# Kernel optimization log

Measured on AMD Instinct MI355X. Metric: run time of the kernel, lower is better.

Reference implementation:

```python
import jax, jax.numpy as jnp
import numpy as np
import math

QUERY_LEN = 64
VALUES_LEN = 64
NUM_HEADS = 16


def setup_inputs() -> dict:
    key = jax.random.key(0)
    k1, k2, k3, k4 = jax.random.split(key, 4)
    B, G, N = 2, 4, 1024
    D = QUERY_LEN * NUM_HEADS  # 1024
    queries = jax.random.normal(k1, (B, G, N, D), dtype=jnp.float32)
    keys = jax.random.normal(k2, (B, G, N, D), dtype=jnp.float32)
    values = jax.random.normal(k3, (B, G, N, VALUES_LEN * NUM_HEADS), dtype=jnp.float32)
    neuron_bank_connectivity_sub = jax.random.uniform(k4, (1, G, 1, N, N), dtype=jnp.float32)
    return {
        "queries": queries,
        "keys": keys,
        "values": values,
        "neuron_bank_connectivity_sub": neuron_bank_connectivity_sub,
    }


def reference(queries, keys, values, neuron_bank_connectivity_sub):
    B, G, N, _ = queries.shape
    H, dq, dv = NUM_HEADS, QUERY_LEN, VALUES_LEN
    # view last dim as (vec_len, num_heads), move heads forward: [B,G,H,N,d]
    q = queries.reshape(B, G, N, dq, H).transpose(0, 1, 4, 2, 3)
    k = keys.reshape(B, G, N, dq, H).transpose(0, 1, 4, 2, 3)
    v = values.reshape(B, G, N, dv, H).transpose(0, 1, 4, 2, 3)
    scores = jnp.einsum('bghnd,bghmd->bghnm', q, k) / math.sqrt(dq)
    probs = jax.nn.softmax(scores - neuron_bank_connectivity_sub, axis=-1)
    out = jnp.einsum('bghnm,bghmd->bghnd', probs, v)  # [B,G,H,N,dv]
    # Faithful to original: view() applied to the contiguous [B,G,H,N,dv] buffer
    return out.reshape(B, G, N, H * dv)
```

## Files before the change

### kernel.cpp

```cpp
#include <hip/hip_runtime.h>
#include <hip/hip_bf16.h>
#include <math.h>

#define B_ 2
#define G_ 4
#define N_ 1024
#define H_ 16
#define D_ 64
#define BG_ (B_*G_)
#define BGH_ (B_*G_*H_)
#define MK 64
#define LOG2E 1.44269504f
#define QSCALE (0.125f * LOG2E)

typedef __bf16 bf16;
typedef bf16 bf16x8 __attribute__((ext_vector_type(8)));
typedef bf16 bf16x2 __attribute__((ext_vector_type(2)));
typedef float f32x4 __attribute__((ext_vector_type(4)));
typedef float f32x16 __attribute__((ext_vector_type(16)));
typedef int i32x4 __attribute__((ext_vector_type(4)));
typedef unsigned u32x2 __attribute__((ext_vector_type(2)));

static __device__ __forceinline__ f32x16 mfma32(bf16x8 a, bf16x8 b, f32x16 c) {
    return __builtin_amdgcn_mfma_f32_32x32x16_bf16(a, b, c, 0, 0, 0);
}

static __device__ __forceinline__ unsigned pk2(float a, float b) {
    bf16x2 t; t[0] = (bf16)a; t[1] = (bf16)b;
    return __builtin_bit_cast(unsigned, t);
}

static __device__ __forceinline__ void pl32swap(unsigned& a, unsigned& b, int hi) {
#if __has_builtin(__builtin_amdgcn_permlane32_swap)
    u32x2 r = __builtin_amdgcn_permlane32_swap(a, b, false, false);
    a = r[0]; b = r[1];
    (void)hi;
#else
    unsigned ax = (unsigned)__shfl_xor((int)a, 32, 64);
    unsigned bx = (unsigned)__shfl_xor((int)b, 32, 64);
    unsigned na = hi ? bx : a;
    unsigned nb = hi ? b : ax;
    a = na; b = nb;
#endif
}

static __device__ __forceinline__ void gll16(const void* gsrc, void* ldst, int lane) {
#if __has_builtin(__builtin_amdgcn_global_load_lds)
    (void)lane;
    __builtin_amdgcn_global_load_lds((const __attribute__((address_space(1))) void*)gsrc,
                                     (__attribute__((address_space(3))) void*)ldst, 16, 0, 0);
#else
    *(bf16x8*)((bf16*)ldst + lane * 8) = *(const bf16x8*)((const bf16*)gsrc);
#endif
}

#define HS 1160
#define NS 72

__global__ __launch_bounds__(256) void transpose_fused(
    const float* __restrict__ q, const float* __restrict__ k, const float* __restrict__ v,
    const float* __restrict__ bias,
    bf16* __restrict__ qt, bf16* __restrict__ ktb, bf16* __restrict__ vtT16,
    float* __restrict__ biasX)
{
    __shared__ __attribute__((aligned(16))) bf16 lds[16 * HS];
    int bx = blockIdx.x;
    int t = threadIdx.x;

    if (bx >= 3 * 512) {
        int idx = bx - 3 * 512;
        int gg  = idx >> 8;
        int tl  = idx & 255;
        int q0  = (tl >> 4) * 64;
        int m0  = (tl & 15) * 64;
        float* ldsF = (float*)lds;

        int mi = t & 15, qr = t >> 4;
#pragma unroll
        for (int rr = 0; rr < 4; ++rr) {
            int row = qr + rr * 16;
            f32x4 val = *(const f32x4*)(bias + ((size_t)(gg * N_ + q0 + row) * N_ + m0 + 4 * mi));
            *(f32x4*)(&ldsF[row * 68 + 4 * mi]) = val;
        }
        __syncthreads();
        int qr2 = t & 63, mb0 = t >> 6;
#pragma unroll
        for (int kk = 0; kk < 4; ++kk) {
            int mbi = mb0 + kk * 4;
            f32x4 vv = *(const f32x4*)(&ldsF[qr2 * 68 + 4 * mbi]);
            *(f32x4*)(biasX + (((size_t)gg * 256 + m0 / 4 + mbi) * N_ + q0 + qr2) * 4) = vv;
        }
        return;
    }

    int tensor = bx >> 9;
    int rr = bx & 511;
    int bg = rr >> 6;
    int tile = rr & 63;
    int n0 = tile * 16;

    const float* src = (tensor == 0) ? q : (tensor == 1) ? k : v;
    float scale = (tensor == 0) ? QSCALE : 1.0f;
    const float* sb = src + (size_t)bg * N_ * 1024 + (size_t)n0 * 1024;

    int h0 = 4 * (t & 3);
    int d  = t >> 2;
    int wbase = h0 * HS + d;
#pragma unroll 4
    for (int i = 0; i < 16; ++i) {
        float4 val = ((const float4*)(sb + (size_t)i * 1024))[t];
        bf16* p = &lds[wbase + i * NS];
        p[0]        = (bf16)(val.x * scale);
        p[HS]       = (bf16)(val.y * scale);
        p[2 * HS]   = (bf16)(val.z * scale);
        p[3 * HS]   = (bf16)(val.w * scale);
    }
    __syncthreads();

    if (tensor < 2) {
        bf16* dst = (tensor == 0) ? qt : ktb;
        int n  = (t >> 3) & 15;
        int db = t & 7;
        int hb = t >> 7;
#pragma unroll
        for (int i = 0; i < 8; ++i) {
            int h = 2 * i + hb;
            bf16x8 vv = *(const bf16x8*)(&lds[h * HS + n * NS + db * 8]);
            *(bf16x8*)(dst + (((size_t)(bg * H_ + h)) * N_ + n0 + n) * D_ + db * 8) = vv;
        }
    } else {
        int dd = t & 63;
        int hb = t >> 6;
#pragma unroll
        for (int i = 0; i < 4; ++i) {
            int h = hb * 4 + i;
            bf16x8 v0, v1;
#pragma unroll
            for (int jj = 0; jj < 8; ++jj) v0[jj] = lds[h * HS + jj * NS + dd];
#pragma unroll
            for (int jj = 0; jj < 8; ++jj) v1[jj] = lds[h * HS + (8 + jj) * NS + dd];
            bf16* dst = vtT16 + (((size_t)(bg * H_ + h) * 64 + tile) * D_ + dd) * 16;
            *(bf16x8*)dst       = v0;
            *(bf16x8*)(dst + 8) = v1;
        }
    }
}

__global__ __launch_bounds__(256, 3) void flash_kernel(
    const bf16* __restrict__ qt, const bf16* __restrict__ kt, const bf16* __restrict__ vtT16,
    const float* __restrict__ biasX, float* __restrict__ out)
{
    __shared__ __attribute__((aligned(16))) bf16 k_lds[2][MK][D_];
    __shared__ __attribute__((aligned(16))) bf16 v_lds[2][D_][MK];

    int tid  = threadIdx.x;
    int w    = tid >> 6;
    int lane = tid & 63;
    int hi   = lane >> 5;
    int q31  = lane & 31;
    int key8 = (q31 & 7) << 3;
    int hi8  = hi << 3;

    int wg   = blockIdx.x;
    int xcd  = wg & 7;
    int slot = wg >> 3;
    int bgh  = xcd * 16 + (slot >> 3);
    int n0   = (slot & 7) * 128;
    int g    = (bgh >> 4) & (G_ - 1);

    const bf16* qb_base = qt + ((size_t)bgh * N_ + n0 + w * 32 + q31) * D_ + hi * 8;
    bf16x8 qb[4];
#pragma unroll
    for (int c = 0; c < 4; ++c) qb[c] = *(const bf16x8*)(qb_base + c * 16);

    f32x16 acc0 = {0,0,0,0,0,0,0,0,0,0,0,0,0,0,0,0};
    f32x16 acc1 = {0,0,0,0,0,0,0,0,0,0,0,0,0,0,0,0};
    float l = 0.f;

    int rloc = lane >> 3;
    int c16  = lane & 7;
    int csw  = c16 ^ rloc;
    bool isK = (w < 2);
    int wrow = (w & 1) * 32;
    const bf16* ksrc = kt + (size_t)bgh * N_ * D_ + (size_t)(wrow + rloc) * D_ + csw * 8;
    const bf16* vsrc = vtT16 + (((size_t)bgh * 64 + (csw >> 1)) * D_ + (wrow + rloc)) * 16 + (csw & 1) * 8;

    const float* bb = biasX + (size_t)g * (256u * 1024 * 4) + (size_t)(n0 + w * 32 + q31) * 4;

    if (isK) {
#pragma unroll
        for (int i = 0; i < 4; ++i) gll16(ksrc + (size_t)i * 8 * D_, &k_lds[0][wrow + i * 8][0], lane);
    } else {
#pragma unroll
        for (int i = 0; i < 4; ++i) gll16(vsrc + (size_t)i * 128, &v_lds[0][wrow + i * 8][0], lane);
    }
    f32x4 bnx[8];
#pragma unroll
    for (int tt = 0; tt < 2; ++tt)
#pragma unroll
        for (int u = 0; u < 4; ++u)
            bnx[tt * 4 + u] = *(const f32x4*)(bb + (size_t)(tt * 8 + 2 * u + hi) * 4096);

    for (int it = 0; it < N_ / MK; ++it) {
        int  cur  = it & 1;
        bool more = (it + 1 < N_ / MK);
        __syncthreads();

        if (more) {
            int nxt = cur ^ 1;
            if (isK) {
                const bf16* ks = ksrc + (size_t)(it + 1) * MK * D_;
#pragma unroll
                for (int i = 0; i < 4; ++i) gll16(ks + (size_t)i * 8 * D_, &k_lds[nxt][wrow + i * 8][0], lane);
            } else {
                const bf16* vs = vsrc + (size_t)(it + 1) * 4096;
#pragma unroll
                for (int i = 0; i < 4; ++i) gll16(vs + (size_t)i * 128, &v_lds[nxt][wrow + i * 8][0], lane);
            }
        }

        f32x16 s0 = {0,0,0,0,0,0,0,0,0,0,0,0,0,0,0,0};
        f32x16 s1 = {0,0,0,0,0,0,0,0,0,0,0,0,0,0,0,0};
        __builtin_amdgcn_s_setprio(1);
#pragma unroll
        for (int c = 0; c < 4; ++c) {
            int off = ((c << 4) | hi8) ^ key8;
            bf16x8 kb0 = *(const bf16x8*)(&k_lds[cur][q31][off]);
            bf16x8 kb1 = *(const bf16x8*)(&k_lds[cur][32 + q31][off]);
            s0 = mfma32(kb0, qb[c], s0);
            s1 = mfma32(kb1, qb[c], s1);
        }
        __builtin_amdgcn_s_setprio(0);

        unsigned wa[2][4], wb[2][4];
#pragma unroll
        for (int tt = 0; tt < 2; ++tt) {
#pragma unroll
            for (int u = 0; u < 4; ++u) {
                const f32x16& s = tt ? s1 : s0;
                f32x4 bvv = bnx[tt * 4 + u];
                float p0 = __builtin_amdgcn_exp2f(__builtin_fmaf(-LOG2E, bvv[0], s[4*u+0]));
                float p1 = __builtin_amdgcn_exp2f(__builtin_fmaf(-LOG2E, bvv[1], s[4*u+1]));
                float p2 = __builtin_amdgcn_exp2f(__builtin_fmaf(-LOG2E, bvv[2], s[4*u+2]));
                float p3 = __builtin_amdgcn_exp2f(__builtin_fmaf(-LOG2E, bvv[3], s[4*u+3]));
                l += (p0 + p1) + (p2 + p3);
                wa[tt][u] = pk2(p0, p1);
                wb[tt][u] = pk2(p2, p3);
            }
        }

        if (more) {
#pragma unroll
            for (int tt = 0; tt < 2; ++tt)
#pragma unroll
                for (int u = 0; u < 4; ++u)
                    bnx[tt * 4 + u] = *(const f32x4*)(bb + (size_t)((it + 1) * 16 + tt * 8 + 2 * u + hi) * 4096);
        }

#pragma unroll
        for (int tt = 0; tt < 2; ++tt) {
            pl32swap(wa[tt][0], wa[tt][1], hi);
            pl32swap(wb[tt][0], wb[tt][1], hi);
            pl32swap(wa[tt][2], wa[tt][3], hi);
            pl32swap(wb[tt][2], wb[tt][3], hi);
        }

        __builtin_amdgcn_s_setprio(1);
#pragma unroll
        for (int tt = 0; tt < 2; ++tt)
#pragma unroll
            for (int c01 = 0; c01 < 2; ++c01) {
                int kc = tt * 2 + c01;
                i32x4 bwi = { (int)wa[tt][2*c01], (int)wb[tt][2*c01],
                              (int)wa[tt][2*c01+1], (int)wb[tt][2*c01+1] };
                bf16x8 pb = __builtin_bit_cast(bf16x8, bwi);
                int off = ((kc << 4) | hi8) ^ key8;
                bf16x8 va0 = *(const bf16x8*)(&v_lds[cur][q31][off]);
                bf16x8 va1 = *(const bf16x8*)(&v_lds[cur][32 + q31][off]);
                acc0 = mfma32(va0, pb, acc0);
                acc1 = mfma32(va1, pb, acc1);
            }
        __builtin_amdgcn_s_setprio(0);
    }

    l += __shfl_xor(l, 32, 64);
    float inv = 1.0f / l;

    float* ob = out + ((size_t)bgh * N_ + n0 + w * 32 + q31) * D_ + hi * 4;
#pragma unroll
    for (int td = 0; td < 2; ++td) {
        const f32x16& a = td ? acc1 : acc0;
#pragma unroll
        for (int u = 0; u < 4; ++u) {
            f32x4 o = { a[4*u+0] * inv, a[4*u+1] * inv, a[4*u+2] * inv, a[4*u+3] * inv };
            *(f32x4*)(ob + td * 32 + u * 8) = o;
        }
    }
}

__global__ __launch_bounds__(256) void naive_kernel(
    const float* __restrict__ q, const float* __restrict__ k,
    const float* __restrict__ v, const float* __restrict__ bias,
    float* __restrict__ out)
{
    __shared__ float sc[N_];
    __shared__ float red[256];
    __shared__ float qrow[64];
    int n = blockIdx.x;
    int bgh = blockIdx.y;
    int bg = bgh >> 4, h = bgh & 15;
    int g = bg & (G_ - 1);
    int tid = threadIdx.x;
    const float* qr = q + ((size_t)(bg * N_ + n)) * 1024;
    if (tid < 64) qrow[tid] = qr[tid * 16 + h];
    __syncthreads();
    const float* bb = bias + (size_t)g * N_ * N_ + (size_t)n * N_;
    for (int m = tid; m < N_; m += 256) {
        const float* kr = k + ((size_t)(bg * N_ + m)) * 1024 + h;
        float dot = 0.f;
        for (int d = 0; d < 64; ++d) dot += qrow[d] * kr[d * 16];
        sc[m] = dot * 0.125f - bb[m];
    }
    __syncthreads();
    float mx = -INFINITY;
    for (int m = tid; m < N_; m += 256) mx = fmaxf(mx, sc[m]);
    red[tid] = mx; __syncthreads();
    for (int s = 128; s > 0; s >>= 1) {
        if (tid < s) red[tid] = fmaxf(red[tid], red[tid + s]);
        __syncthreads();
    }
    float M = red[0]; __syncthreads();
    float sum = 0.f;
    for (int m = tid; m < N_; m += 256) { float e = __expf(sc[m] - M); sc[m] = e; sum += e; }
    red[tid] = sum; __syncthreads();
    for (int s = 128; s > 0; s >>= 1) {
        if (tid < s) red[tid] += red[tid + s];
        __syncthreads();
    }
    float L = red[0]; __syncthreads();
    int d = tid & 63, quarter = tid >> 6;
    float acc = 0.f;
    const float* vb = v + (size_t)bg * N_ * 1024 + d * 16 + h;
    for (int m = quarter * 256; m < quarter * 256 + 256; ++m) acc += sc[m] * vb[(size_t)m * 1024];
    red[tid] = acc; __syncthreads();
    if (tid < 64) {
        float o = (red[tid] + red[tid + 64] + red[tid + 128] + red[tid + 192]) / L;
        out[((size_t)bgh * N_ + n) * 64 + d] = o;
    }
}

extern "C" void kernel_launch(void* const* d_in, const int* in_sizes, int n_in,
                              void* d_out, int out_size, void* d_ws, size_t ws_size,
                              hipStream_t stream) {
    const float* q    = (const float*)d_in[0];
    const float* k    = (const float*)d_in[1];
    const float* v    = (const float*)d_in[2];
    const float* bias = (const float*)d_in[3];
    float* out = (float*)d_out;

    const size_t elems = (size_t)BGH_ * N_ * D_;
    const size_t needA = 3 * elems * sizeof(bf16);
    const size_t need  = needA + (size_t)G_ * N_ * N_ * 4;

    if (ws_size >= need) {
        bf16* qt    = (bf16*)d_ws;
        bf16* ktb   = qt + elems;
        bf16* vtT16 = ktb + elems;
        float* biasX = (float*)((char*)d_ws + needA);
        transpose_fused<<<3 * 512 + 1024, 256, 0, stream>>>(q, k, v, bias, qt, ktb, vtT16, biasX);
        flash_kernel<<<dim3(1024), 256, 0, stream>>>(qt, ktb, vtT16, biasX, out);
    } else {
        dim3 grid(N_, BGH_);
        naive_kernel<<<grid, 256, 0, stream>>>(q, k, v, bias, out);
    }
}
```

Before: 210.0 us.

## Process 64 query rows per wave to reuse K/V LDS loads

Each wave now handles two 32-row query groups (256 rows per block), so every K and V fragment read from LDS feeds two MFMAs instead of one. The key tile is processed in two 32-key halves to bound register pressure. The grid shrinks from 1024 to 512 blocks and launch bounds drop to 2 waves-per-SIMD occupancy. This halves K/V staging traffic per query, at the cost of more registers, lower occupancy, and fewer blocks to fill the GPU.

```diff
diff --git a/kernel.cpp b/kernel.cpp
--- a/kernel.cpp
+++ b/kernel.cpp
@@ -146,7 +146,7 @@
     }
 }
 
-__global__ __launch_bounds__(256, 3) void flash_kernel(
+__global__ __launch_bounds__(256, 2) void flash_kernel(
     const bf16* __restrict__ qt, const bf16* __restrict__ kt, const bf16* __restrict__ vtT16,
     const float* __restrict__ biasX, float* __restrict__ out)
 {
@@ -164,18 +164,25 @@
     int wg   = blockIdx.x;
     int xcd  = wg & 7;
     int slot = wg >> 3;
-    int bgh  = xcd * 16 + (slot >> 3);
-    int n0   = (slot & 7) * 128;
+    int bgh  = xcd * 16 + (slot >> 2);
+    int n0   = (slot & 3) * 256;
     int g    = (bgh >> 4) & (G_ - 1);
 
-    const bf16* qb_base = qt + ((size_t)bgh * N_ + n0 + w * 32 + q31) * D_ + hi * 8;
-    bf16x8 qb[4];
-#pragma unroll
-    for (int c = 0; c < 4; ++c) qb[c] = *(const bf16x8*)(qb_base + c * 16);
-
-    f32x16 acc0 = {0,0,0,0,0,0,0,0,0,0,0,0,0,0,0,0};
-    f32x16 acc1 = {0,0,0,0,0,0,0,0,0,0,0,0,0,0,0,0};
-    float l = 0.f;
+    int qbase = n0 + w * 64;
+
+    const bf16* qb_base = qt + ((size_t)bgh * N_ + qbase + q31) * D_ + hi * 8;
+    bf16x8 qA[4], qB[4];
+#pragma unroll
+    for (int c = 0; c < 4; ++c) {
+        qA[c] = *(const bf16x8*)(qb_base + c * 16);
+        qB[c] = *(const bf16x8*)(qb_base + 32 * D_ + c * 16);
+    }
+
+    f32x16 acc00 = {0,0,0,0,0,0,0,0,0,0,0,0,0,0,0,0};
+    f32x16 acc01 = {0,0,0,0,0,0,0,0,0,0,0,0,0,0,0,0};
+    f32x16 acc10 = {0,0,0,0,0,0,0,0,0,0,0,0,0,0,0,0};
+    f32x16 acc11 = {0,0,0,0,0,0,0,0,0,0,0,0,0,0,0,0};
+    float l0 = 0.f, l1 = 0.f;
 
     int rloc = lane >> 3;
     int c16  = lane & 7;
@@ -185,7 +192,7 @@
     const bf16* ksrc = kt + (size_t)bgh * N_ * D_ + (size_t)(wrow + rloc) * D_ + csw * 8;
     const bf16* vsrc = vtT16 + (((size_t)bgh * 64 + (csw >> 1)) * D_ + (wrow + rloc)) * 16 + (csw & 1) * 8;
 
-    const float* bb = biasX + (size_t)g * (256u * 1024 * 4) + (size_t)(n0 + w * 32 + q31) * 4;
+    const float* bb = biasX + (size_t)g * (256u * 4096) + (size_t)(qbase + q31) * 4;
 
     if (isK) {
 #pragma unroll
@@ -194,12 +201,14 @@
 #pragma unroll
         for (int i = 0; i < 4; ++i) gll16(vsrc + (size_t)i * 128, &v_lds[0][wrow + i * 8][0], lane);
     }
-    f32x4 bnx[8];
-#pragma unroll
-    for (int tt = 0; tt < 2; ++tt)
-#pragma unroll
-        for (int u = 0; u < 4; ++u)
-            bnx[tt * 4 + u] = *(const f32x4*)(bb + (size_t)(tt * 8 + 2 * u + hi) * 4096);
+    f32x4 bvA[2][4], bvB[2][4];
+#pragma unroll
+    for (int g01 = 0; g01 < 2; ++g01)
+#pragma unroll
+        for (int u = 0; u < 4; ++u) {
+            bvA[g01][u] = *(const f32x4*)(bb + g01 * 128 + (size_t)(2 * u + hi) * 4096);
+            bvB[g01][u] = *(const f32x4*)(bb + g01 * 128 + (size_t)(8 + 2 * u + hi) * 4096);
+        }
 
     for (int it = 0; it < N_ / MK; ++it) {
         int  cur  = it & 1;
@@ -219,81 +228,151 @@
             }
         }
 
-        f32x16 s0 = {0,0,0,0,0,0,0,0,0,0,0,0,0,0,0,0};
-        f32x16 s1 = {0,0,0,0,0,0,0,0,0,0,0,0,0,0,0,0};
-        __builtin_amdgcn_s_setprio(1);
-#pragma unroll
-        for (int c = 0; c < 4; ++c) {
-            int off = ((c << 4) | hi8) ^ key8;
-            bf16x8 kb0 = *(const bf16x8*)(&k_lds[cur][q31][off]);
-            bf16x8 kb1 = *(const bf16x8*)(&k_lds[cur][32 + q31][off]);
-            s0 = mfma32(kb0, qb[c], s0);
-            s1 = mfma32(kb1, qb[c], s1);
-        }
-        __builtin_amdgcn_s_setprio(0);
-
-        unsigned wa[2][4], wb[2][4];
-#pragma unroll
-        for (int tt = 0; tt < 2; ++tt) {
-#pragma unroll
-            for (int u = 0; u < 4; ++u) {
-                const f32x16& s = tt ? s1 : s0;
-                f32x4 bvv = bnx[tt * 4 + u];
-                float p0 = __builtin_amdgcn_exp2f(__builtin_fmaf(-LOG2E, bvv[0], s[4*u+0]));
-                float p1 = __builtin_amdgcn_exp2f(__builtin_fmaf(-LOG2E, bvv[1], s[4*u+1]));
-                float p2 = __builtin_amdgcn_exp2f(__builtin_fmaf(-LOG2E, bvv[2], s[4*u+2]));
-                float p3 = __builtin_amdgcn_exp2f(__builtin_fmaf(-LOG2E, bvv[3], s[4*u+3]));
-                l += (p0 + p1) + (p2 + p3);
-                wa[tt][u] = pk2(p0, p1);
-                wb[tt][u] = pk2(p2, p3);
-            }
-        }
-
-        if (more) {
-#pragma unroll
-            for (int tt = 0; tt < 2; ++tt)
-#pragma unroll
-                for (int u = 0; u < 4; ++u)
-                    bnx[tt * 4 + u] = *(const f32x4*)(bb + (size_t)((it + 1) * 16 + tt * 8 + 2 * u + hi) * 4096);
-        }
-
-#pragma unroll
-        for (int tt = 0; tt < 2; ++tt) {
-            pl32swap(wa[tt][0], wa[tt][1], hi);
-            pl32swap(wb[tt][0], wb[tt][1], hi);
-            pl32swap(wa[tt][2], wa[tt][3], hi);
-            pl32swap(wb[tt][2], wb[tt][3], hi);
-        }
-
-        __builtin_amdgcn_s_setprio(1);
-#pragma unroll
-        for (int tt = 0; tt < 2; ++tt)
+        {
+            f32x16 s0 = {0,0,0,0,0,0,0,0,0,0,0,0,0,0,0,0};
+            f32x16 s1 = {0,0,0,0,0,0,0,0,0,0,0,0,0,0,0,0};
+            __builtin_amdgcn_s_setprio(1);
+#pragma unroll
+            for (int c = 0; c < 4; ++c) {
+                int off = ((c << 4) | hi8) ^ key8;
+                bf16x8 kb = *(const bf16x8*)(&k_lds[cur][q31][off]);
+                s0 = mfma32(kb, qA[c], s0);
+                s1 = mfma32(kb, qB[c], s1);
+            }
+            __builtin_amdgcn_s_setprio(0);
+
+            unsigned wa[2][4], wb[2][4];
+#pragma unroll
+            for (int g01 = 0; g01 < 2; ++g01) {
+#pragma unroll
+                for (int u = 0; u < 4; ++u) {
+                    const f32x16& s = g01 ? s1 : s0;
+                    f32x4 bvv = bvA[g01][u];
+                    float p0 = __builtin_amdgcn_exp2f(__builtin_fmaf(-LOG2E, bvv[0], s[4*u+0]));
+                    float p1 = __builtin_amdgcn_exp2f(__builtin_fmaf(-LOG2E, bvv[1], s[4*u+1]));
+                    float p2 = __builtin_amdgcn_exp2f(__builtin_fmaf(-LOG2E, bvv[2], s[4*u+2]));
+                    float p3 = __builtin_amdgcn_exp2f(__builtin_fmaf(-LOG2E, bvv[3], s[4*u+3]));
+                    if (g01) l1 += (p0 + p1) + (p2 + p3); else l0 += (p0 + p1) + (p2 + p3);
+                    wa[g01][u] = pk2(p0, p1);
+                    wb[g01][u] = pk2(p2, p3);
+                }
+            }
+
+            if (more) {
+#pragma unroll
+                for (int g01 = 0; g01 < 2; ++g01)
+#pragma unroll
+                    for (int u = 0; u < 4; ++u)
+                        bvA[g01][u] = *(const f32x4*)(bb + g01 * 128 + (size_t)((it + 1) * 16 + 2 * u + hi) * 4096);
+            }
+
+#pragma unroll
+            for (int g01 = 0; g01 < 2; ++g01) {
+                pl32swap(wa[g01][0], wa[g01][1], hi);
+                pl32swap(wb[g01][0], wb[g01][1], hi);
+                pl32swap(wa[g01][2], wa[g01][3], hi);
+                pl32swap(wb[g01][2], wb[g01][3], hi);
+            }
+
+            __builtin_amdgcn_s_setprio(1);
 #pragma unroll
             for (int c01 = 0; c01 < 2; ++c01) {
-                int kc = tt * 2 + c01;
-                i32x4 bwi = { (int)wa[tt][2*c01], (int)wb[tt][2*c01],
-                              (int)wa[tt][2*c01+1], (int)wb[tt][2*c01+1] };
-                bf16x8 pb = __builtin_bit_cast(bf16x8, bwi);
-                int off = ((kc << 4) | hi8) ^ key8;
+                int off = ((c01 << 4) | hi8) ^ key8;
                 bf16x8 va0 = *(const bf16x8*)(&v_lds[cur][q31][off]);
                 bf16x8 va1 = *(const bf16x8*)(&v_lds[cur][32 + q31][off]);
-                acc0 = mfma32(va0, pb, acc0);
-                acc1 = mfma32(va1, pb, acc1);
-            }
-        __builtin_amdgcn_s_setprio(0);
-    }
-
-    l += __shfl_xor(l, 32, 64);
-    float inv = 1.0f / l;
-
-    float* ob = out + ((size_t)bgh * N_ + n0 + w * 32 + q31) * D_ + hi * 4;
-#pragma unroll
-    for (int td = 0; td < 2; ++td) {
-        const f32x16& a = td ? acc1 : acc0;
-#pragma unroll
-        for (int u = 0; u < 4; ++u) {
-            f32x4 o = { a[4*u+0] * inv, a[4*u+1] * inv, a[4*u+2] * inv, a[4*u+3] * inv };
-            *(f32x4*)(ob + td * 32 + u * 8) = o;
+                i32x4 b0 = { (int)wa[0][2*c01], (int)wb[0][2*c01], (int)wa[0][2*c01+1], (int)wb[0][2*c01+1] };
+                i32x4 b1 = { (int)wa[1][2*c01], (int)wb[1][2*c01], (int)wa[1][2*c01+1], (int)wb[1][2*c01+1] };
+                bf16x8 pb0 = __builtin_bit_cast(bf16x8, b0);
+                bf16x8 pb1 = __builtin_bit_cast(bf16x8, b1);
+                acc00 = mfma32(va0, pb0, acc00);
+                acc01 = mfma32(va1, pb0, acc01);
+                acc10 = mfma32(va0, pb1, acc10);
+                acc11 = mfma32(va1, pb1, acc11);
+            }
+            __builtin_amdgcn_s_setprio(0);
+        }
+
+        {
+            f32x16 s0 = {0,0,0,0,0,0,0,0,0,0,0,0,0,0,0,0};
+            f32x16 s1 = {0,0,0,0,0,0,0,0,0,0,0,0,0,0,0,0};
+            __builtin_amdgcn_s_setprio(1);
+#pragma unroll
+            for (int c = 0; c < 4; ++c) {
+                int off = ((c << 4) | hi8) ^ key8;
+                bf16x8 kb = *(const bf16x8*)(&k_lds[cur][32 + q31][off]);
+                s0 = mfma32(kb, qA[c], s0);
+                s1 = mfma32(kb, qB[c], s1);
+            }
+            __builtin_amdgcn_s_setprio(0);
+
+            unsigned wa[2][4], wb[2][4];
+#pragma unroll
+            for (int g01 = 0; g01 < 2; ++g01) {
+#pragma unroll
+                for (int u = 0; u < 4; ++u) {
+                    const f32x16& s = g01 ? s1 : s0;
+                    f32x4 bvv = bvB[g01][u];
+                    float p0 = __builtin_amdgcn_exp2f(__builtin_fmaf(-LOG2E, bvv[0], s[4*u+0]));
+                    float p1 = __builtin_amdgcn_exp2f(__builtin_fmaf(-LOG2E, bvv[1], s[4*u+1]));
+                    float p2 = __builtin_amdgcn_exp2f(__builtin_fmaf(-LOG2E, bvv[2], s[4*u+2]));
+                    float p3 = __builtin_amdgcn_exp2f(__builtin_fmaf(-LOG2E, bvv[3], s[4*u+3]));
+                    if (g01) l1 += (p0 + p1) + (p2 + p3); else l0 += (p0 + p1) + (p2 + p3);
+                    wa[g01][u] = pk2(p0, p1);
+                    wb[g01][u] = pk2(p2, p3);
+                }
+            }
+
+            if (more) {
+#pragma unroll
+                for (int g01 = 0; g01 < 2; ++g01)
+#pragma unroll
+                    for (int u = 0; u < 4; ++u)
+                        bvB[g01][u] = *(const f32x4*)(bb + g01 * 128 + (size_t)((it + 1) * 16 + 8 + 2 * u + hi) * 4096);
+            }
+
+#pragma unroll
+            for (int g01 = 0; g01 < 2; ++g01) {
+                pl32swap(wa[g01][0], wa[g01][1], hi);
+                pl32swap(wb[g01][0], wb[g01][1], hi);
+                pl32swap(wa[g01][2], wa[g01][3], hi);
+                pl32swap(wb[g01][2], wb[g01][3], hi);
+            }
+
+            __builtin_amdgcn_s_setprio(1);
+#pragma unroll
+            for (int c01 = 0; c01 < 2; ++c01) {
+                int off = (((2 + c01) << 4) | hi8) ^ key8;
+                bf16x8 va0 = *(const bf16x8*)(&v_lds[cur][q31][off]);
+                bf16x8 va1 = *(const bf16x8*)(&v_lds[cur][32 + q31][off]);
+                i32x4 b0 = { (int)wa[0][2*c01], (int)wb[0][2*c01], (int)wa[0][2*c01+1], (int)wb[0][2*c01+1] };
+                i32x4 b1 = { (int)wa[1][2*c01], (int)wb[1][2*c01], (int)wa[1][2*c01+1], (int)wb[1][2*c01+1] };
+                bf16x8 pb0 = __builtin_bit_cast(bf16x8, b0);
+                bf16x8 pb1 = __builtin_bit_cast(bf16x8, b1);
+                acc00 = mfma32(va0, pb0, acc00);
+                acc01 = mfma32(va1, pb0, acc01);
+                acc10 = mfma32(va0, pb1, acc10);
+                acc11 = mfma32(va1, pb1, acc11);
+            }
+            __builtin_amdgcn_s_setprio(0);
+        }
+    }
+
+    l0 += __shfl_xor(l0, 32, 64);
+    l1 += __shfl_xor(l1, 32, 64);
+    float inv0 = 1.0f / l0, inv1 = 1.0f / l1;
+
+#pragma unroll
+    for (int g01 = 0; g01 < 2; ++g01) {
+        float inv = g01 ? inv1 : inv0;
+        float* ob = out + ((size_t)bgh * N_ + qbase + g01 * 32 + q31) * D_ + hi * 4;
+#pragma unroll
+        for (int td = 0; td < 2; ++td) {
+            const f32x16& a = g01 ? (td ? acc11 : acc10) : (td ? acc01 : acc00);
+#pragma unroll
+            for (int u = 0; u < 4; ++u) {
+                f32x4 o = { a[4*u+0] * inv, a[4*u+1] * inv, a[4*u+2] * inv, a[4*u+3] * inv };
+                *(f32x4*)(ob + td * 32 + u * 8) = o;
+            }
         }
     }
 }
@@ -368,7 +447,7 @@
         bf16* vtT16 = ktb + elems;
         float* biasX = (float*)((char*)d_ws + needA);
         transpose_fused<<<3 * 512 + 1024, 256, 0, stream>>>(q, k, v, bias, qt, ktb, vtT16, biasX);
-        flash_kernel<<<dim3(1024), 256, 0, stream>>>(qt, ktb, vtT16, biasX, out);
+        flash_kernel<<<dim3(512), 256, 0, stream>>>(qt, ktb, vtT16, biasX, out);
     } else {
         dim3 grid(N_, BGH_);
         naive_kernel<<<grid, 256, 0, stream>>>(q, k, v, bias, out);
```

Result: slower. 225.5 us (+7.4%).
